# Performance work log

Hardware: AMD Instinct MI355X
Metric: run time of the kernel (lower is better)

The kernel has to match this reference:

```python
import jax, jax.numpy as jnp
import numpy as np

EMBED_DIM = 1024
NUM_HEADS = 8
PROJ_DIM = EMBED_DIM // NUM_HEADS  # 128
SIGMA = 1.0        # attn_param
DISP = 1           # attn_displacement
BATCH = 8
SEQ_LEN = 2048
# per-head hard-coded attention positions (length == num_heads)
POSITIONS = ['center', 'left', 'right', 'first', 'last', 'center', 'left', 'right']


def _head_centers(L):
    """Center of the analytic Gaussian per head and per query position. [H, L]"""
    i = jnp.arange(L, dtype=jnp.float32)
    centers = []
    for pos in POSITIONS:
        if pos == 'center':
            c = i
        elif pos == 'left':
            c = i - DISP
        elif pos == 'right':
            c = i + DISP
        elif pos == 'first':
            c = jnp.zeros_like(i)
        else:  # 'last' (no padding: last valid index is L-1)
            c = jnp.full_like(i, L - 1)
        centers.append(c)
    return jnp.stack(centers)  # [H, L]


def setup_inputs() -> dict:
    key = jax.random.key(0)
    k1, k2, k3 = jax.random.split(key, 3)
    x = jax.random.normal(k1, (BATCH, SEQ_LEN, EMBED_DIM), dtype=jnp.float32)
    # xavier-ish scale for square weights
    s = (6.0 / (EMBED_DIM + EMBED_DIM)) ** 0.5
    W_in = jax.random.uniform(k2, (EMBED_DIM, EMBED_DIM), dtype=jnp.float32, minval=-s, maxval=s)
    W_out = jax.random.uniform(k3, (EMBED_DIM, EMBED_DIM), dtype=jnp.float32, minval=-s, maxval=s)
    return {"x": x, "W_in": W_in, "W_out": W_out}


def reference(x, W_in, W_out):
    B, L, E = x.shape
    H, P = NUM_HEADS, PROJ_DIM
    # value projection (F.linear with input_weights), split into heads
    v = (x @ W_in.T).reshape(B, L, H, P).transpose(0, 2, 1, 3)  # [B, H, L, P]
    # analytic per-head attention weights: Gaussian in key-position around center
    j = jnp.arange(L, dtype=jnp.float32)
    c = _head_centers(L)                                         # [H, Lq]
    logits = -((j[None, None, :] - c[:, :, None]) ** 2) / (2.0 * SIGMA ** 2)  # [H, Lq, Lk]
    w = jax.nn.softmax(logits, axis=-1)                          # [H, Lq, Lk]
    # weighted value aggregation (torch.bmm(attn_weights, values) per head)
    attended = jnp.einsum('hqk,bhkp->bhqp', w, v)                # [B, H, L, P]
    attended = attended.transpose(0, 2, 1, 3).reshape(B, L, E)
    # bias-free output projection
    return attended @ W_out.T
```

## Files before the change

### kernel.cpp

```cpp
#include <hip/hip_runtime.h>
#include <stdint.h>

typedef unsigned short u16;
typedef unsigned int   u32;

typedef float  f32x4  __attribute__((ext_vector_type(4)));
typedef __bf16 bf16x8 __attribute__((ext_vector_type(8)));

template <int V> struct ic { static constexpr int value = V; };

__device__ __forceinline__ u16 f2bf(float f) {
  union { float f; u32 u; } c; c.f = f;
  u32 u = c.u + 0x7fffu + ((c.u >> 16) & 1u);
  return (u16)(u >> 16);
}
__device__ __forceinline__ float bf2f(u16 h) {
  union { u32 u; float f; } c; c.u = ((u32)h) << 16;
  return c.f;
}
__device__ __forceinline__ void gll16(const void* g, void* l) {
  __builtin_amdgcn_global_load_lds(
      (const __attribute__((address_space(1))) void*)g,
      (__attribute__((address_space(3))) void*)l, 16, 0, 0);
}

__global__ __launch_bounds__(256)
void cvt_all(const float4* __restrict__ x,  uint2* __restrict__ xb,  int n4x,
             const float4* __restrict__ wi, uint2* __restrict__ wib,
             const float4* __restrict__ wo, uint2* __restrict__ wob, int n4w) {
  int i = blockIdx.x * 256 + threadIdx.x;
  const float4* s; uint2* d; int j;
  if (i < n4x)            { s = x;  d = xb;  j = i; }
  else if (i < n4x + n4w) { s = wi; d = wib; j = i - n4x; }
  else                    { s = wo; d = wob; j = i - n4x - n4w; }
  float4 v = s[j];
  uint2 o;
  o.x = (u32)f2bf(v.x) | ((u32)f2bf(v.y) << 16);
  o.y = (u32)f2bf(v.z) | ((u32)f2bf(v.w) << 16);
  d[j] = o;
}

template <bool OUT_BF16>
__global__ __launch_bounds__(512, 2)
void gemm_nt_256(const u16* __restrict__ A, const u16* __restrict__ B,
                 void* __restrict__ Cout, int M, int N, int K) {
  __shared__ u16 Ls[65536];
  const int tid  = threadIdx.x;
  const int lane = tid & 63;
  const int wave = tid >> 6;
  const int wm   = wave >> 2;
  const int wn   = wave & 3;
  const int ml   = lane & 15;
  const int q    = lane >> 4;
  const int pc   = q ^ ((ml >> 2) & 3);

  const int flat = blockIdx.y * 4 + blockIdx.x;
  const int xcd  = flat & 7;
  const int slot = flat >> 3;
  const int mt   = xcd * (gridDim.y >> 3) + (slot >> 2);
  const int nt   = slot & 3;
  const int m0   = mt * 256;
  const int n0   = nt * 256;

  const int g    = (tid & 3) ^ ((tid >> 4) & 3);
  const int srow = tid >> 2;
  const u16* Ag = A + (size_t)(m0 + srow) * K + g * 8;
  const u16* Bg = B + (size_t)(n0 + srow) * K + g * 8;
  char* LsB = (char*)Ls;
  const int wb = wave * 1024;

  auto stageA = [&](int bufsel, int s, int k0) {
    char* lb = LsB + (size_t)(bufsel * 4 + s) * 16384 + wb;
    gll16(Ag + k0 + s * 32, lb);
    gll16(Ag + (size_t)128 * K + k0 + s * 32, lb + 8192);
  };
  auto stageB = [&](int bufsel, int s, int k0) {
    char* lb = LsB + (size_t)(bufsel * 4 + 2 + s) * 16384 + wb;
    gll16(Bg + k0 + s * 32, lb);
    gll16(Bg + (size_t)128 * K + k0 + s * 32, lb + 8192);
  };

  f32x4  acc[8][4] = {};
  bf16x8 bfv[2][4];
  const int aoff = (wm * 128 + ml) * 32 + pc * 8;
  const int boff = (wn * 64 + ml) * 32 + pc * 8;

  auto phase = [&](auto MHc, auto Sc, auto RDBc, int buf) {
    constexpr int MH = MHc.value;
    constexpr int S  = Sc.value;
    __builtin_amdgcn_s_barrier();
    __builtin_amdgcn_sched_barrier(0);
    const u16* Ab = Ls + (size_t)(buf * 4 + S) * 8192;
    const u16* Bb = Ls + (size_t)(buf * 4 + 2 + S) * 8192;
    bf16x8 a[4];
#pragma unroll
    for (int i = 0; i < 4; ++i)
      a[i] = *reinterpret_cast<const bf16x8*>(&Ab[aoff + MH * 2048 + i * 512]);
    if constexpr (RDBc.value != 0) {
#pragma unroll
      for (int j = 0; j < 4; ++j)
        bfv[S][j] = *reinterpret_cast<const bf16x8*>(&Bb[boff + j * 512]);
    }
    __builtin_amdgcn_s_setprio(1);
#pragma unroll
    for (int i = 0; i < 4; ++i)
#pragma unroll
      for (int j = 0; j < 4; ++j)
        acc[MH * 4 + i][j] = __builtin_amdgcn_mfma_f32_16x16x32_bf16(
            a[i], bfv[S][j], acc[MH * 4 + i][j], 0, 0, 0);
    __builtin_amdgcn_s_setprio(0);
  };

  stageA(0, 0, 0); stageB(0, 0, 0); stageA(0, 1, 0); stageB(0, 1, 0);

  const int NT = K >> 6;
  int buf = 0;
  for (int t = 0; t < NT - 1; ++t, buf ^= 1) {
    const int kn = (t + 1) << 6;
    stageA(buf ^ 1, 0, kn);
    asm volatile("s_waitcnt vmcnt(6)" ::: "memory");
    phase(ic<0>{}, ic<0>{}, ic<1>{}, buf);
    stageB(buf ^ 1, 0, kn);
    asm volatile("s_waitcnt vmcnt(4)" ::: "memory");
    phase(ic<0>{}, ic<1>{}, ic<1>{}, buf);
    stageA(buf ^ 1, 1, kn);
    phase(ic<1>{}, ic<0>{}, ic<0>{}, buf);
    stageB(buf ^ 1, 1, kn);
    phase(ic<1>{}, ic<1>{}, ic<0>{}, buf);
  }
  asm volatile("s_waitcnt vmcnt(4)" ::: "memory");
  phase(ic<0>{}, ic<0>{}, ic<1>{}, buf);
  asm volatile("s_waitcnt vmcnt(0)" ::: "memory");
  phase(ic<0>{}, ic<1>{}, ic<1>{}, buf);
  phase(ic<1>{}, ic<0>{}, ic<0>{}, buf);
  phase(ic<1>{}, ic<1>{}, ic<0>{}, buf);

  const int rowb = m0 + wm * 128 + q * 4;
  const int colb = n0 + wn * 64 + ml;
#pragma unroll
  for (int mf = 0; mf < 8; ++mf)
#pragma unroll
    for (int nf = 0; nf < 4; ++nf)
#pragma unroll
      for (int r = 0; r < 4; ++r) {
        size_t idx = (size_t)(rowb + mf * 16 + r) * N + (colb + nf * 16);
        float val = acc[mf][nf][r];
        if (OUT_BF16) ((u16*)Cout)[idx] = f2bf(val);
        else          ((float*)Cout)[idx] = val;
      }
}

__global__ __launch_bounds__(256)
void gauss_conv(const u16* __restrict__ v, u16* __restrict__ att, int L) {
  constexpr float wt[13] = {
    1.5229979744712628e-08f, 3.7266531720786709e-06f, 3.3546262790251185e-04f,
    1.1108996538242306e-02f, 1.3533528323661270e-01f, 6.0653065971263342e-01f,
    1.0f,
    6.0653065971263342e-01f, 1.3533528323661270e-01f, 1.1108996538242306e-02f,
    3.3546262790251185e-04f, 3.7266531720786709e-06f, 1.5229979744712628e-08f
  };
  const int t  = threadIdx.x;
  const int fg = t & 15;
  const int li = t >> 4;
  const int l  = blockIdx.x * 16 + li;
  const int h  = blockIdx.y;
  const int b  = blockIdx.z;
  int c;
  switch (h) {
    case 0: case 5: c = l;     break;
    case 1: case 6: c = l - 1; break;
    case 2: case 7: c = l + 1; break;
    case 3:         c = 0;     break;
    default:        c = L - 1; break;
  }
  const int fbase = h * 128 + fg * 8;
  const u16* vb = v + (size_t)b * L * 1024 + fbase;

  float a[8] = {};
  float Z = 0.f;
#pragma unroll
  for (int d = -6; d <= 6; ++d) {
    int idx = c + d;
    bool ok = (idx >= 0) && (idx < L);
    int ic_ = idx < 0 ? 0 : (idx >= L ? L - 1 : idx);
    float w = ok ? wt[d + 6] : 0.f;
    Z += w;
    uint4 p = *reinterpret_cast<const uint4*>(vb + (size_t)ic_ * 1024);
    a[0] = fmaf(w, bf2f((u16)(p.x & 0xffffu)), a[0]);
    a[1] = fmaf(w, bf2f((u16)(p.x >> 16)),     a[1]);
    a[2] = fmaf(w, bf2f((u16)(p.y & 0xffffu)), a[2]);
    a[3] = fmaf(w, bf2f((u16)(p.y >> 16)),     a[3]);
    a[4] = fmaf(w, bf2f((u16)(p.z & 0xffffu)), a[4]);
    a[5] = fmaf(w, bf2f((u16)(p.z >> 16)),     a[5]);
    a[6] = fmaf(w, bf2f((u16)(p.w & 0xffffu)), a[6]);
    a[7] = fmaf(w, bf2f((u16)(p.w >> 16)),     a[7]);
  }
  float inv = 1.0f / Z;
  uint4 o;
  o.x = (u32)f2bf(a[0] * inv) | ((u32)f2bf(a[1] * inv) << 16);
  o.y = (u32)f2bf(a[2] * inv) | ((u32)f2bf(a[3] * inv) << 16);
  o.z = (u32)f2bf(a[4] * inv) | ((u32)f2bf(a[5] * inv) << 16);
  o.w = (u32)f2bf(a[6] * inv) | ((u32)f2bf(a[7] * inv) << 16);
  *reinterpret_cast<uint4*>(att + (size_t)(b * L + l) * 1024 + fbase) = o;
}

extern "C" void kernel_launch(void* const* d_in, const int* in_sizes, int n_in,
                              void* d_out, int out_size, void* d_ws, size_t ws_size,
                              hipStream_t stream) {
  const int Bb = 8, L = 2048, E = 1024;
  const int M = Bb * L, N = E, K = E;

  const float* x  = (const float*)d_in[0];
  const float* Wi = (const float*)d_in[1];
  const float* Wo = (const float*)d_in[2];
  float* out = (float*)d_out;

  size_t offV  = (size_t)M * E * 2;
  size_t offWi = offV + (size_t)M * E * 2;
  size_t offWo = offWi + (size_t)E * E * 2;
  size_t need  = offWo + (size_t)E * E * 2;
  if (ws_size < need) return;

  u16* xb  = (u16*)d_ws;
  u16* v   = (u16*)((char*)d_ws + offV);
  u16* wib = (u16*)((char*)d_ws + offWi);
  u16* wob = (u16*)((char*)d_ws + offWo);
  u16* att = xb;

  int n4x = M * E / 4, n4w = E * E / 4;
  int nblk = (n4x + 2 * n4w) / 256;
  cvt_all<<<nblk, 256, 0, stream>>>((const float4*)x, (uint2*)xb, n4x,
                                    (const float4*)Wi, (uint2*)wib,
                                    (const float4*)Wo, (uint2*)wob, n4w);

  dim3 gg(N / 256, M / 256);
  gemm_nt_256<true ><<<gg, 512, 0, stream>>>(xb,  wib, v,   M, N, K);
  gauss_conv<<<dim3(L / 16, 8, Bb), 256, 0, stream>>>(v, att, L);
  gemm_nt_256<false><<<gg, 512, 0, stream>>>(att, wob, out, M, N, K);
}
```

Before: 210.7 us.

## Restructure GEMM main loop with register double-buffered fragments and deeper prefetch

Rewrites the bf16 GEMM mainloop so that A/B fragments are double-buffered in registers, letting LDS reads for the next sub-phase overlap the current MFMA block. Global-to-LDS staging now runs two k-tiles ahead, and the LDS layout changes to 64-element-wide rows with a new XOR swizzle. The aim is to hide LDS and global load latency behind MFMAs and reduce stalls at barriers. The cost is higher register pressure from the extra fragment buffers, along with the risk that the new swizzle causes bank conflicts or that the wait counts are miscounted.

```diff
diff --git a/kernel.cpp b/kernel.cpp
--- a/kernel.cpp
+++ b/kernel.cpp
@@ -6,8 +6,6 @@
 
 typedef float  f32x4  __attribute__((ext_vector_type(4)));
 typedef __bf16 bf16x8 __attribute__((ext_vector_type(8)));
-
-template <int V> struct ic { static constexpr int value = V; };
 
 __device__ __forceinline__ u16 f2bf(float f) {
   union { float f; u32 u; } c; c.f = f;
@@ -52,7 +50,7 @@
   const int wn   = wave & 3;
   const int ml   = lane & 15;
   const int q    = lane >> 4;
-  const int pc   = q ^ ((ml >> 2) & 3);
+  const int qs   = q ^ (((ml >> 2) & 1) << 1);
 
   const int flat = blockIdx.y * 4 + blockIdx.x;
   const int xcd  = flat & 7;
@@ -62,78 +60,89 @@
   const int m0   = mt * 256;
   const int n0   = nt * 256;
 
-  const int g    = (tid & 3) ^ ((tid >> 4) & 3);
-  const int srow = tid >> 2;
-  const u16* Ag = A + (size_t)(m0 + srow) * K + g * 8;
-  const u16* Bg = B + (size_t)(n0 + srow) * K + g * 8;
+  const int srr = tid >> 3;
+  const int gc  = (tid & 7) ^ (((tid >> 5) & 1) << 1);
+  const u16* Agb = A + (size_t)(m0 + srr) * K + gc * 8;
+  const u16* Bgb = B + (size_t)(n0 + srr) * K + gc * 8;
   char* LsB = (char*)Ls;
-  const int wb = wave * 1024;
-
-  auto stageA = [&](int bufsel, int s, int k0) {
-    char* lb = LsB + (size_t)(bufsel * 4 + s) * 16384 + wb;
-    gll16(Ag + k0 + s * 32, lb);
-    gll16(Ag + (size_t)128 * K + k0 + s * 32, lb + 8192);
-  };
-  auto stageB = [&](int bufsel, int s, int k0) {
-    char* lb = LsB + (size_t)(bufsel * 4 + 2 + s) * 16384 + wb;
-    gll16(Bg + k0 + s * 32, lb);
-    gll16(Bg + (size_t)128 * K + k0 + s * 32, lb + 8192);
-  };
+  const int wlds = wave * 1024;
+
+  auto stageA = [&](int bufb, int h, int k0) {
+    char* d = LsB + bufb + h * 16384 + wlds;
+    gll16(Agb + (size_t)(h * 128) * K + k0, d);
+    gll16(Agb + (size_t)(h * 128 + 64) * K + k0, d + 8192);
+  };
+  auto stageB = [&](int bufb, int h, int k0) {
+    char* d = LsB + bufb + 32768 + h * 16384 + wlds;
+    gll16(Bgb + (size_t)(h * 128) * K + k0, d);
+    gll16(Bgb + (size_t)(h * 128 + 64) * K + k0, d + 8192);
+  };
+
+  const int aB_ = wm * 8192 + ml * 64 + qs * 8;
+  const int bB_ = 16384 + (wn >> 1) * 8192 + ((wn & 1) * 64 + ml) * 64 + qs * 8;
 
   f32x4  acc[8][4] = {};
-  bf16x8 bfv[2][4];
-  const int aoff = (wm * 128 + ml) * 32 + pc * 8;
-  const int boff = (wn * 64 + ml) * 32 + pc * 8;
-
-  auto phase = [&](auto MHc, auto Sc, auto RDBc, int buf) {
-    constexpr int MH = MHc.value;
-    constexpr int S  = Sc.value;
+  bf16x8 fa0[4], fa1[4], B0[4], B1[4];
+
+  auto rdA = [&](bf16x8* dst, int bw, int MH, int s) {
+#pragma unroll
+    for (int i = 0; i < 4; ++i)
+      dst[i] = *reinterpret_cast<const bf16x8*>(&Ls[bw + aB_ + MH * 4096 + i * 1024 + s * 32]);
+  };
+  auto rdB = [&](bf16x8* dst, int bw, int s) {
+#pragma unroll
+    for (int j = 0; j < 4; ++j)
+      dst[j] = *reinterpret_cast<const bf16x8*>(&Ls[bw + bB_ + j * 1024 + s * 32]);
+  };
+  auto mfma16 = [&](int mh, const bf16x8* a, const bf16x8* b) {
+    __builtin_amdgcn_s_setprio(1);
+#pragma unroll
+    for (int i = 0; i < 4; ++i)
+#pragma unroll
+      for (int j = 0; j < 4; ++j)
+        acc[mh * 4 + i][j] = __builtin_amdgcn_mfma_f32_16x16x32_bf16(
+            a[i], b[j], acc[mh * 4 + i][j], 0, 0, 0);
+    __builtin_amdgcn_s_setprio(0);
+  };
+  auto barrier = [&] {
+    __builtin_amdgcn_sched_barrier(0);
     __builtin_amdgcn_s_barrier();
-    __builtin_amdgcn_sched_barrier(0);
-    const u16* Ab = Ls + (size_t)(buf * 4 + S) * 8192;
-    const u16* Bb = Ls + (size_t)(buf * 4 + 2 + S) * 8192;
-    bf16x8 a[4];
-#pragma unroll
-    for (int i = 0; i < 4; ++i)
-      a[i] = *reinterpret_cast<const bf16x8*>(&Ab[aoff + MH * 2048 + i * 512]);
-    if constexpr (RDBc.value != 0) {
-#pragma unroll
-      for (int j = 0; j < 4; ++j)
-        bfv[S][j] = *reinterpret_cast<const bf16x8*>(&Bb[boff + j * 512]);
-    }
-    __builtin_amdgcn_s_setprio(1);
-#pragma unroll
-    for (int i = 0; i < 4; ++i)
-#pragma unroll
-      for (int j = 0; j < 4; ++j)
-        acc[MH * 4 + i][j] = __builtin_amdgcn_mfma_f32_16x16x32_bf16(
-            a[i], bfv[S][j], acc[MH * 4 + i][j], 0, 0, 0);
-    __builtin_amdgcn_s_setprio(0);
-  };
-
-  stageA(0, 0, 0); stageB(0, 0, 0); stageA(0, 1, 0); stageB(0, 1, 0);
+  };
+
+  stageB(0, 0, 0);      stageB(0, 1, 0);
+  stageA(0, 0, 0);      stageA(0, 1, 0);
+  stageB(65536, 0, 64); stageB(65536, 1, 64);
+  stageA(65536, 0, 64); stageA(65536, 1, 64);
+  asm volatile("s_waitcnt vmcnt(8)" ::: "memory");
+  barrier();
+  rdA(fa0, 0, 0, 0);
+  rdB(B0, 0, 0);
 
   const int NT = K >> 6;
-  int buf = 0;
-  for (int t = 0; t < NT - 1; ++t, buf ^= 1) {
-    const int kn = (t + 1) << 6;
-    stageA(buf ^ 1, 0, kn);
-    asm volatile("s_waitcnt vmcnt(6)" ::: "memory");
-    phase(ic<0>{}, ic<0>{}, ic<1>{}, buf);
-    stageB(buf ^ 1, 0, kn);
-    asm volatile("s_waitcnt vmcnt(4)" ::: "memory");
-    phase(ic<0>{}, ic<1>{}, ic<1>{}, buf);
-    stageA(buf ^ 1, 1, kn);
-    phase(ic<1>{}, ic<0>{}, ic<0>{}, buf);
-    stageB(buf ^ 1, 1, kn);
-    phase(ic<1>{}, ic<1>{}, ic<0>{}, buf);
+  int bufb = 0;
+  for (int t = 0; t < NT; ++t, bufb ^= 65536) {
+    const int  bw     = bufb >> 1;
+    const int  bwn    = (bufb ^ 65536) >> 1;
+    const bool rdnext = (t + 1 < NT);
+    const bool stg    = (t + 2 < NT);
+    const int  kst    = (t + 2) << 6;
+    mfma16(0, fa0, B0);
+    rdA(fa1, bw, 0, 1); rdB(B1, bw, 1);
+    barrier();
+    mfma16(0, fa1, B1);
+    rdA(fa0, bw, 1, 0);
+    if (stg) { stageB(bufb, 0, kst); stageB(bufb, 1, kst); }
+    barrier();
+    mfma16(1, fa0, B0);
+    rdA(fa1, bw, 1, 1);
+    if (stg)         { asm volatile("s_waitcnt vmcnt(4)" ::: "memory"); }
+    else if (rdnext) { asm volatile("s_waitcnt vmcnt(0)" ::: "memory"); }
+    barrier();
+    mfma16(1, fa1, B1);
+    if (rdnext) { rdA(fa0, bwn, 0, 0); rdB(B0, bwn, 0); }
+    if (stg) { stageA(bufb, 0, kst); stageA(bufb, 1, kst); }
+    barrier();
   }
-  asm volatile("s_waitcnt vmcnt(4)" ::: "memory");
-  phase(ic<0>{}, ic<0>{}, ic<1>{}, buf);
-  asm volatile("s_waitcnt vmcnt(0)" ::: "memory");
-  phase(ic<0>{}, ic<1>{}, ic<1>{}, buf);
-  phase(ic<1>{}, ic<0>{}, ic<0>{}, buf);
-  phase(ic<1>{}, ic<1>{}, ic<0>{}, buf);
 
   const int rowb = m0 + wm * 128 + q * 4;
   const int colb = n0 + wn * 64 + ml;
```

New measurement: 207.3 us. About the same (-1.6%).
